# Performance work log

Hardware: AMD Instinct MI355X
Metric: run time of the kernel (lower is better)

The kernel has to match this reference:

```python
import math
import jax, jax.numpy as jnp
import numpy as np

# hard-coded constants from the source module
SPIRAL_AMP, SPIRAL_PHASE, SPIRAL_SLOPE, SPIRAL_OFFSET = 3.5, 0.0, 0.15, 0.0
MAX_DIGITS, VOCAB_SIZE, POS_DIM, TOK_DIM, QK_DIM = 10, 10, 3, 2, 4

# position map (length 34): source table id and row index within that table
_SRC = np.array([0]*10 + [2] + [0]*10 + [2] + [0]*10 + [1, 2], dtype=np.int32)
_IDX = np.array(list(range(10)) + [0] + list(range(10)) + [1] + list(range(10)) + [0, 2], dtype=np.int32)
# tables are concatenated as [digit(10), z_hi(1), special(3)] -> row offsets per source id
_OFFS = np.array([0, 10, 11], dtype=np.int32)


def _rmsnorm(x, w):
    return x / jnp.sqrt(jnp.mean(x * x, axis=-1, keepdims=True) + 1e-5) * w


def setup_inputs() -> dict:
    key = jax.random.key(0)
    ks = jax.random.split(key, 9)
    B, T = 65536, 34
    idx = jax.random.randint(ks[0], (B, T), 0, VOCAB_SIZE, dtype=jnp.int32)
    return {
        "idx": idx,
        "tok_arc_A": jnp.asarray(2.5, jnp.float32),
        "tok_arc_start": jnp.asarray(-1.2, jnp.float32),
        "tok_arc_stride": jnp.asarray(0.29, jnp.float32),
        "z_hi_pos": 0.1 * jax.random.normal(ks[1], (1, POS_DIM), jnp.float32),
        "special_pos_equals": 0.1 * jax.random.normal(ks[2], (1, POS_DIM), jnp.float32),
        "q_proj_w": 0.5 * jax.random.normal(ks[3], (QK_DIM, POS_DIM), jnp.float32),
        "q_phase_angle": 0.1 * jax.random.normal(ks[4], (1,), jnp.float32),
        "out_proj_A": 0.5 * jax.random.normal(ks[5], (5, 1), jnp.float32),
        "out_proj_B": 0.5 * jax.random.normal(ks[6], (1, 5), jnp.float32),
        "norm_weight": jnp.ones((5,), jnp.float32),
        "fc1_w": 0.5 * jax.random.normal(ks[7], (2, 5), jnp.float32),
        "head_proj_w": 0.5 * jax.random.normal(ks[8], (TOK_DIM, 5), jnp.float32),
    }


def reference(idx, tok_arc_A, tok_arc_start, tok_arc_stride, z_hi_pos,
              special_pos_equals, q_proj_w, q_phase_angle, out_proj_A,
              out_proj_B, norm_weight, fc1_w, head_proj_w):
    B, T = idx.shape
    # token embedding table [V, 2] on an arc
    d = jnp.arange(VOCAB_SIZE, dtype=jnp.float32)
    ang = tok_arc_start + d * tok_arc_stride
    tok_table = tok_arc_A * jnp.stack([jnp.cos(ang), jnp.sin(ang)], axis=1)
    # digit positions on a spiral [10, 3]
    i = jnp.arange(MAX_DIGITS, dtype=jnp.float32)
    a = 2.0 * math.pi * i / MAX_DIGITS + SPIRAL_PHASE
    digit_pos = jnp.stack([SPIRAL_AMP * jnp.cos(a), SPIRAL_AMP * jnp.sin(a),
                           SPIRAL_SLOPE * i + SPIRAL_OFFSET], axis=1)
    special_pos = jnp.concatenate([jnp.zeros((1, POS_DIM)), special_pos_equals,
                                   jnp.zeros((1, POS_DIM))], axis=0)
    full_table = jnp.concatenate([digit_pos, z_hi_pos, special_pos], axis=0)  # [14,3]
    flat = jnp.asarray(_OFFS)[jnp.asarray(_SRC[:T])] + jnp.asarray(_IDX[:T])
    pos = full_table[flat]                                   # [T, 3]

    tok = tok_table[idx]                                     # [B, T, 2]
    x = jnp.concatenate([tok, jnp.broadcast_to(pos[None], (B, T, POS_DIM))], axis=-1)
    h = _rmsnorm(x, norm_weight)
    tok_h, pos_h = h[..., :TOK_DIM], h[..., TOK_DIM:]

    q = pos_h @ q_proj_w.T                                   # [B, T, 4]
    k = q                                                    # identical projection
    v = tok_h @ head_proj_w                                  # [B, T, 5]
    # phase rotation on even/odd pairs of q
    c, s = jnp.cos(q_phase_angle[0]), jnp.sin(q_phase_angle[0])
    q0, q1 = q[..., 0::2], q[..., 1::2]
    q = jnp.stack([q0 * c - q1 * s, q0 * s + q1 * c], axis=-1).reshape(q.shape)

    att = jnp.einsum('btd,bsd->bts', q, k) / math.sqrt(QK_DIM)
    mask = jnp.tril(jnp.ones((T, T), bool))
    att = jax.nn.softmax(jnp.where(mask, att, -jnp.inf), axis=-1)
    out = jnp.einsum('bts,bsh->bth', att, v)                 # [B, T, 5]

    x = x + out @ out_proj_A @ out_proj_B
    ffn = jax.nn.gelu(_rmsnorm(x, norm_weight) @ fc1_w.T, approximate=False)
    x = x + ffn @ head_proj_w
    return (_rmsnorm(x, norm_weight) @ head_proj_w.T) @ tok_table.T  # [B, T, 10]
```

## Files before the change

### kernel.cpp

```cpp
#include <hip/hip_runtime.h>
#include <math.h>

#define T34 34

#define PW_OFF  0
#define TOK_OFF 1260
#define POS_OFF 1280
#define HA_OFF  1420

__global__ __launch_bounds__(64) void prep_kernel(
    const float* __restrict__ pA, const float* __restrict__ pStart,
    const float* __restrict__ pStride, const float* __restrict__ zhi,
    const float* __restrict__ spe, const float* __restrict__ qw,
    const float* __restrict__ qph, const float* __restrict__ opA,
    const float* __restrict__ wn, const float* __restrict__ H,
    float* __restrict__ ws)
{
    __shared__ float sK[T34][4];
    __shared__ float sInv[T34];
    const int t = blockIdx.x;
    const int s = threadIdx.x;
    const float A = pA[0];

    if (s < T34) {
        float p0 = 0.f, p1 = 0.f, p2 = 0.f;
        if (s == 21)      { p0 = spe[0]; p1 = spe[1]; p2 = spe[2]; }
        else if (s == 32) { p0 = zhi[0]; p1 = zhi[1]; p2 = zhi[2]; }
        else if (s != 10 && s != 33) {
            int i = (s < 10) ? s : (s < 21 ? s - 11 : s - 22);
            float a = 0.62831853071795864769f * (float)i;
            p0 = 3.5f * cosf(a); p1 = 3.5f * sinf(a); p2 = 0.15f * (float)i;
        }
        float inv = rsqrtf((A*A + p0*p0 + p1*p1 + p2*p2) * 0.2f + 1e-5f);
        float c0 = p0 * wn[2], c1 = p1 * wn[3], c2 = p2 * wn[4];
        #pragma unroll
        for (int j = 0; j < 4; ++j)
            sK[s][j] = (c0*qw[j*3+0] + c1*qw[j*3+1] + c2*qw[j*3+2]) * inv;
        sInv[s] = inv;
        if (s == t) {
            ws[POS_OFF + 4*t + 0] = p0;
            ws[POS_OFF + 4*t + 1] = p1;
            ws[POS_OFF + 4*t + 2] = p2;
            ws[POS_OFF + 4*t + 3] = 0.f;
        }
    }
    __syncthreads();

    float cc = cosf(qph[0]), sn = sinf(qph[0]);
    float k0 = sK[t][0], k1 = sK[t][1], k2 = sK[t][2], k3 = sK[t][3];
    float q0 = k0*cc - k1*sn, q1 = k0*sn + k1*cc;
    float q2 = k2*cc - k3*sn, q3 = k2*sn + k3*cc;

    float e = 0.f;
    if (s <= t && s < T34) {
        float d = 0.5f*(q0*sK[s][0] + q1*sK[s][1] + q2*sK[s][2] + q3*sK[s][3]);
        e = expf(d);
    }
    float Z = e;
    #pragma unroll
    for (int off = 1; off < 64; off <<= 1) Z += __shfl_xor(Z, off);
    if (s < 36) ws[PW_OFF + t*36 + s] = (s <= t && s < T34) ? (e / Z) * sInv[s] : 0.f;

    if (t == 0) {
        if (s < 36) ws[PW_OFF + 34*36 + s] = 0.f;
        if (s < 10) {
            float ang = pStart[0] + (float)s * pStride[0];
            ws[TOK_OFF + 2*s + 0] = A * cosf(ang);
            ws[TOK_OFF + 2*s + 1] = A * sinf(ang);
        } else if (s == 10) {
            float a0 = 0.f, a1 = 0.f;
            #pragma unroll
            for (int h = 0; h < 5; ++h) { a0 += H[h]*opA[h]; a1 += H[5+h]*opA[h]; }
            ws[HA_OFF + 0] = a0 * wn[0];
            ws[HA_OFF + 1] = a1 * wn[1];
        } else if (s == 11) {
            ws[POS_OFF + 4*34 + 0] = 0.f;
            ws[POS_OFF + 4*34 + 1] = 0.f;
            ws[POS_OFF + 4*34 + 2] = 0.f;
            ws[POS_OFF + 4*34 + 3] = 0.f;
        }
    }
}

__global__ __launch_bounds__(448) void micro_kernel(
    const int*  __restrict__ idx,
    const float* __restrict__ pA, const float* __restrict__ pStart,
    const float* __restrict__ pStride,
    const float* __restrict__ opB, const float* __restrict__ wn,
    const float* __restrict__ fc1, const float* __restrict__ H,
    const float* __restrict__ ws,
    float* __restrict__ out)
{
    __shared__ unsigned su[64*36];
    __shared__ float    pr[64*35*2];
    __shared__ float    stk[20];
    __shared__ unsigned lut[10];
    const int lane = threadIdx.x;
    const int ty   = threadIdx.y;
    const int tid  = ty*64 + lane;
    const int b0   = blockIdx.x << 6;

    if (tid < 20) stk[tid] = ws[TOK_OFF + tid];
    if (tid >= 64 && tid < 74) {
        int d = tid - 64;
        float ang = pStart[0] + (float)d * pStride[0];
        float ux = pA[0]*__cosf(ang), uy = pA[0]*__sinf(ang);
        unsigned hx = (__float_as_uint(ux) + 0x8000u) >> 16;
        unsigned hy = (__float_as_uint(uy) + 0x8000u) & 0xffff0000u;
        lut[d] = hy | hx;
    }
    if (tid < 128) su[(tid >> 1)*36 + 34 + (tid & 1)] = 0u;
    __syncthreads();

    {
        const int4* src4 = (const int4*)(idx + (size_t)b0*T34);
        for (int e4 = tid; e4 < 544; e4 += 448) {
            int4 d4 = src4[e4];
            int e = e4 << 2;
            #pragma unroll
            for (int k = 0; k < 4; ++k) {
                int d = (k==0) ? d4.x : (k==1) ? d4.y : (k==2) ? d4.z : d4.w;
                int ee = e + k;
                unsigned bp = (unsigned)ee / 34u;
                int s = ee - (int)(bp*34u);
                su[bp*36u + (unsigned)s] = lut[d];
            }
        }
    }
    __syncthreads();

    {
        const int tyu = __builtin_amdgcn_readfirstlane(ty);
        const uint4* __restrict__ srow4 = (const uint4*)(su + lane*36);
        const float* __restrict__ Pb = ws + PW_OFF + tyu*36;

        float mx[5] = {0,0,0,0,0}, my[5] = {0,0,0,0,0};
        #pragma unroll
        for (int s4 = 0; s4 < 9; ++s4) {
            uint4 pk4 = srow4[s4];
            #pragma unroll
            for (int k = 0; k < 4; ++k) {
                unsigned pk = (k==0) ? pk4.x : (k==1) ? pk4.y : (k==2) ? pk4.z : pk4.w;
                float ux = __uint_as_float(pk << 16);
                float uy = __uint_as_float(pk & 0xffff0000u);
                int s = s4*4 + k;
                #pragma unroll
                for (int j = 0; j < 5; ++j) {
                    float P = Pb[j*252 + s];
                    mx[j] = fmaf(P, ux, mx[j]);
                    my[j] = fmaf(P, uy, my[j]);
                }
            }
        }

        const float hA0 = ws[HA_OFF], hA1 = ws[HA_OFF+1];
        const float w0=wn[0], w1=wn[1], w2=wn[2], w3=wn[3], w4=wn[4];
        const float ob0=opB[0], ob1=opB[1], ob2=opB[2], ob3=opB[3], ob4=opB[4];
        const unsigned* __restrict__ srow = su + lane*36;

        #pragma unroll
        for (int j = 0; j < 5; ++j) {
            const int t = tyu + 7*j;
            float g = mx[j]*hA0 + my[j]*hA1;
            unsigned pkt = srow[t];
            float x0 = __uint_as_float(pkt << 16)         + g*ob0;
            float x1 = __uint_as_float(pkt & 0xffff0000u) + g*ob1;
            float x2 = ws[POS_OFF + 4*t + 0] + g*ob2;
            float x3 = ws[POS_OFF + 4*t + 1] + g*ob3;
            float x4 = ws[POS_OFF + 4*t + 2] + g*ob4;

            float inv1 = rsqrtf((x0*x0+x1*x1+x2*x2+x3*x3+x4*x4)*0.2f + 1e-5f);
            float h0=x0*inv1*w0, h1=x1*inv1*w1, h2=x2*inv1*w2, h3=x3*inv1*w3, h4=x4*inv1*w4;
            float z0 = h0*fc1[0]+h1*fc1[1]+h2*fc1[2]+h3*fc1[3]+h4*fc1[4];
            float z1 = h0*fc1[5]+h1*fc1[6]+h2*fc1[7]+h3*fc1[8]+h4*fc1[9];
            float g0 = 0.5f*z0*(1.f + erff(z0*0.70710678118654752440f));
            float g1 = 0.5f*z1*(1.f + erff(z1*0.70710678118654752440f));
            x0 += g0*H[0] + g1*H[5];
            x1 += g0*H[1] + g1*H[6];
            x2 += g0*H[2] + g1*H[7];
            x3 += g0*H[3] + g1*H[8];
            x4 += g0*H[4] + g1*H[9];
            float inv2 = rsqrtf((x0*x0+x1*x1+x2*x2+x3*x3+x4*x4)*0.2f + 1e-5f);
            h0=x0*inv2*w0; h1=x1*inv2*w1; h2=x2*inv2*w2; h3=x3*inv2*w3; h4=x4*inv2*w4;
            float p0 = h0*H[0]+h1*H[1]+h2*H[2]+h3*H[3]+h4*H[4];
            float p1 = h0*H[5]+h1*H[6]+h2*H[7]+h3*H[8]+h4*H[9];
            pr[(lane*35 + t)*2 + 0] = p0;
            pr[(lane*35 + t)*2 + 1] = p1;
        }
    }
    __syncthreads();

    {
        float4* __restrict__ o = (float4*)out + (size_t)b0*85;
        for (int e4 = tid; e4 < 5440; e4 += 448) {
            int bp = e4 / 85;
            int r4 = e4 - 85*bp;
            float4 v;
            #pragma unroll
            for (int k = 0; k < 4; ++k) {
                int f = 4*r4 + k;
                int t = f / 10;
                int c = f - 10*t;
                float p0 = pr[(bp*35 + t)*2 + 0];
                float p1 = pr[(bp*35 + t)*2 + 1];
                ((float*)&v)[k] = p0*stk[2*c] + p1*stk[2*c+1];
            }
            o[e4] = v;
        }
    }
}

extern "C" void kernel_launch(void* const* d_in, const int* in_sizes, int n_in,
                              void* d_out, int out_size, void* d_ws, size_t ws_size,
                              hipStream_t stream)
{
    const int*   idx  = (const int*)  d_in[0];
    const float* pA   = (const float*)d_in[1];
    const float* pSt  = (const float*)d_in[2];
    const float* pSd  = (const float*)d_in[3];
    const float* zhi  = (const float*)d_in[4];
    const float* spe  = (const float*)d_in[5];
    const float* qw   = (const float*)d_in[6];
    const float* qph  = (const float*)d_in[7];
    const float* opA  = (const float*)d_in[8];
    const float* opB  = (const float*)d_in[9];
    const float* wn   = (const float*)d_in[10];
    const float* fc1  = (const float*)d_in[11];
    const float* H    = (const float*)d_in[12];
    float* ws  = (float*)d_ws;
    float* out = (float*)d_out;

    hipLaunchKernelGGL(prep_kernel, dim3(34), dim3(64), 0, stream,
                       pA, pSt, pSd, zhi, spe, qw, qph, opA, wn, H, ws);
    hipLaunchKernelGGL(micro_kernel, dim3(1024), dim3(64, 7), 0, stream,
                       idx, pA, pSt, pSd, opB, wn, fc1, H, ws, out);
}
```

Baseline: 140.2 us.

## Use 512-thread blocks, tanh GELU, and pair-wise output stores

Raises the block size from 7 to 8 waves so each wave handles rows t = ty + 8j, clamping the out-of-range rows to a padding row. The exact erf GELU becomes a tanh approximation built on __expf, which changes numerics slightly. The output stage now has each thread write five consecutive float4s for a pair of positions from a float2 shared buffer, replacing per-element divides. Together these aim to cut ALU cost and indexing overhead, at the price of some redundant work on the clamped padding rows and a small accuracy loss in GELU.

```diff
diff --git a/kernel.cpp b/kernel.cpp
--- a/kernel.cpp
+++ b/kernel.cpp
@@ -82,7 +82,14 @@
     }
 }
 
-__global__ __launch_bounds__(448) void micro_kernel(
+__device__ __forceinline__ float gelu_fast(float z) {
+    float w = 0.7978845608028654f * (z + 0.044715f * z * z * z);
+    float e = __expf(2.f * w);
+    float th = 1.f - 2.f / (e + 1.f);
+    return 0.5f * z * (1.f + th);
+}
+
+__global__ __launch_bounds__(512, 8) void micro_kernel(
     const int*  __restrict__ idx,
     const float* __restrict__ pA, const float* __restrict__ pStart,
     const float* __restrict__ pStride,
@@ -92,12 +99,12 @@
     float* __restrict__ out)
 {
     __shared__ unsigned su[64*36];
-    __shared__ float    pr[64*35*2];
+    __shared__ float2   prv[64*36];
     __shared__ float    stk[20];
     __shared__ unsigned lut[10];
-    const int lane = threadIdx.x;
-    const int ty   = threadIdx.y;
-    const int tid  = ty*64 + lane;
+    const int tid  = threadIdx.x;
+    const int lane = tid & 63;
+    const int ty   = tid >> 6;
     const int b0   = blockIdx.x << 6;
 
     if (tid < 20) stk[tid] = ws[TOK_OFF + tid];
@@ -114,7 +121,7 @@
 
     {
         const int4* src4 = (const int4*)(idx + (size_t)b0*T34);
-        for (int e4 = tid; e4 < 544; e4 += 448) {
+        for (int e4 = tid; e4 < 544; e4 += 512) {
             int4 d4 = src4[e4];
             int e = e4 << 2;
             #pragma unroll
@@ -132,7 +139,12 @@
     {
         const int tyu = __builtin_amdgcn_readfirstlane(ty);
         const uint4* __restrict__ srow4 = (const uint4*)(su + lane*36);
-        const float* __restrict__ Pb = ws + PW_OFF + tyu*36;
+        int row[5];
+        #pragma unroll
+        for (int j = 0; j < 5; ++j) {
+            int t = tyu + 8*j;
+            row[j] = (t < 34) ? t : 34;
+        }
 
         float mx[5] = {0,0,0,0,0}, my[5] = {0,0,0,0,0};
         #pragma unroll
@@ -146,7 +158,7 @@
                 int s = s4*4 + k;
                 #pragma unroll
                 for (int j = 0; j < 5; ++j) {
-                    float P = Pb[j*252 + s];
+                    float P = ws[PW_OFF + row[j]*36 + s];
                     mx[j] = fmaf(P, ux, mx[j]);
                     my[j] = fmaf(P, uy, my[j]);
                 }
@@ -160,21 +172,22 @@
 
         #pragma unroll
         for (int j = 0; j < 5; ++j) {
-            const int t = tyu + 7*j;
+            const int t  = tyu + 8*j;
+            const int rc = row[j];
             float g = mx[j]*hA0 + my[j]*hA1;
-            unsigned pkt = srow[t];
+            unsigned pkt = srow[rc];
             float x0 = __uint_as_float(pkt << 16)         + g*ob0;
             float x1 = __uint_as_float(pkt & 0xffff0000u) + g*ob1;
-            float x2 = ws[POS_OFF + 4*t + 0] + g*ob2;
-            float x3 = ws[POS_OFF + 4*t + 1] + g*ob3;
-            float x4 = ws[POS_OFF + 4*t + 2] + g*ob4;
+            float x2 = ws[POS_OFF + 4*rc + 0] + g*ob2;
+            float x3 = ws[POS_OFF + 4*rc + 1] + g*ob3;
+            float x4 = ws[POS_OFF + 4*rc + 2] + g*ob4;
 
             float inv1 = rsqrtf((x0*x0+x1*x1+x2*x2+x3*x3+x4*x4)*0.2f + 1e-5f);
             float h0=x0*inv1*w0, h1=x1*inv1*w1, h2=x2*inv1*w2, h3=x3*inv1*w3, h4=x4*inv1*w4;
             float z0 = h0*fc1[0]+h1*fc1[1]+h2*fc1[2]+h3*fc1[3]+h4*fc1[4];
             float z1 = h0*fc1[5]+h1*fc1[6]+h2*fc1[7]+h3*fc1[8]+h4*fc1[9];
-            float g0 = 0.5f*z0*(1.f + erff(z0*0.70710678118654752440f));
-            float g1 = 0.5f*z1*(1.f + erff(z1*0.70710678118654752440f));
+            float g0 = gelu_fast(z0);
+            float g1 = gelu_fast(z1);
             x0 += g0*H[0] + g1*H[5];
             x1 += g0*H[1] + g1*H[6];
             x2 += g0*H[2] + g1*H[7];
@@ -184,28 +197,30 @@
             h0=x0*inv2*w0; h1=x1*inv2*w1; h2=x2*inv2*w2; h3=x3*inv2*w3; h4=x4*inv2*w4;
             float p0 = h0*H[0]+h1*H[1]+h2*H[2]+h3*H[3]+h4*H[4];
             float p1 = h0*H[5]+h1*H[6]+h2*H[7]+h3*H[8]+h4*H[9];
-            pr[(lane*35 + t)*2 + 0] = p0;
-            pr[(lane*35 + t)*2 + 1] = p1;
+            if (t < 34) prv[lane*36 + t] = make_float2(p0, p1);
         }
     }
     __syncthreads();
 
     {
-        float4* __restrict__ o = (float4*)out + (size_t)b0*85;
-        for (int e4 = tid; e4 < 5440; e4 += 448) {
-            int bp = e4 / 85;
-            int r4 = e4 - 85*bp;
-            float4 v;
-            #pragma unroll
-            for (int k = 0; k < 4; ++k) {
-                int f = 4*r4 + k;
-                int t = f / 10;
-                int c = f - 10*t;
-                float p0 = pr[(bp*35 + t)*2 + 0];
-                float p1 = pr[(bp*35 + t)*2 + 1];
-                ((float*)&v)[k] = p0*stk[2*c] + p1*stk[2*c+1];
+        float4* __restrict__ o4 = (float4*)out + (size_t)b0*85;
+        for (int e = tid; e < 1088; e += 512) {
+            int bp = e / 17;
+            int sg = e - 17*bp;
+            float2 pa = prv[bp*36 + 2*sg];
+            float2 pb = prv[bp*36 + 2*sg + 1];
+            #pragma unroll
+            for (int k = 0; k < 5; ++k) {
+                float4 v;
+                #pragma unroll
+                for (int c4 = 0; c4 < 4; ++c4) {
+                    int f = 4*k + c4;
+                    float2 p = (f < 10) ? pa : pb;
+                    int c = (f < 10) ? f : f - 10;
+                    ((float*)&v)[c4] = p.x*stk[2*c] + p.y*stk[2*c+1];
+                }
+                o4[bp*85 + sg*5 + k] = v;
             }
-            o[e4] = v;
         }
     }
 }
@@ -232,6 +247,6 @@
 
     hipLaunchKernelGGL(prep_kernel, dim3(34), dim3(64), 0, stream,
                        pA, pSt, pSd, zhi, spe, qw, qph, opA, wn, H, ws);
-    hipLaunchKernelGGL(micro_kernel, dim3(1024), dim3(64, 7), 0, stream,
+    hipLaunchKernelGGL(micro_kernel, dim3(1024), dim3(512), 0, stream,
                        idx, pA, pSt, pSd, opB, wn, fc1, H, ws, out);
 }
```

Measured after the change: 193.4 us. 1.38x slower.
